# Kernel optimization log

Measured on AMD Instinct MI355X. Metric: run time of the kernel, lower is better.

The kernel has to match this reference:

```python
import jax, jax.numpy as jnp
import numpy as np

B, L, D, F = 4096, 200, 64, 100000


def setup_inputs() -> dict:
    key = jax.random.key(0)
    ks = jax.random.split(key, 12)
    film_hist = jax.random.randint(ks[0], (B, L), 0, F)                 # padded rated-film indices
    ratings = jax.random.uniform(ks[1], (B, L), jnp.float32) * 4.5 + 0.5  # letterboxd-style 0.5..5
    lengths = jax.random.randint(ks[2], (B,), 1, L + 1)                 # ragged history lengths (>=1)
    film_indices = jax.random.randint(ks[3], (B,), 0, F)                # target films to score
    emb_table = jax.random.normal(ks[4], (F, D), jnp.float32) * 0.1
    W1 = jax.random.normal(ks[5], (5 * D, 2 * D), jnp.float32) * 0.05
    b1 = jnp.zeros((2 * D,), jnp.float32)
    W2 = jax.random.normal(ks[6], (2 * D, D), jnp.float32) * 0.05
    b2 = jnp.zeros((D,), jnp.float32)
    W3 = jax.random.normal(ks[7], (D, 1), jnp.float32) * 0.05
    b3 = jnp.zeros((1,), jnp.float32)
    return {"film_hist": film_hist, "ratings": ratings, "lengths": lengths,
            "film_indices": film_indices, "emb_table": emb_table,
            "W1": W1, "b1": b1, "W2": W2, "b2": b2, "W3": W3, "b3": b3}


def _user_embeddings(film_hist, ratings, lengths, emb_table):
    # mask[b, l] = l < lengths[b]
    mask = jnp.arange(L)[None, :] < lengths[:, None]          # [B, L]
    n = lengths.astype(jnp.float32)                           # [B]
    mean_r = jnp.sum(jnp.where(mask, ratings, 0.0), axis=1) / n
    weights = ratings - mean_r[:, None] + 0.1                 # [B, L]
    hist_emb = emb_table[film_hist]                           # [B, L, D]
    w = hist_emb * weights[:, :, None]                        # weighted film embeddings
    m3 = mask[:, :, None]
    wmin = jnp.min(jnp.where(m3, w, jnp.inf), axis=1)
    wmax = jnp.max(jnp.where(m3, w, -jnp.inf), axis=1)
    wmean = jnp.sum(jnp.where(m3, w, 0.0), axis=1) / n[:, None]
    # median: sort valid entries (pads go to +inf at the end); torch.median
    # returns the lower middle element -> index (n-1)//2
    ws = jnp.sort(jnp.where(m3, w, jnp.inf), axis=1)
    mid = ((lengths - 1) // 2)[:, None, None]                 # [B,1,1]
    wmed = jnp.take_along_axis(ws, jnp.broadcast_to(mid, (B, 1, D)), axis=1)[:, 0, :]
    ue = jnp.concatenate([wmin, wmax, wmean, wmed], axis=1)   # [B, 4D]
    return ue / jnp.linalg.norm(ue, axis=1, keepdims=True)


def reference(film_hist, ratings, lengths, film_indices, emb_table, W1, b1, W2, b2, W3, b3):
    ue = _user_embeddings(film_hist, ratings, lengths, emb_table)  # [B, 4D]
    fe = emb_table[film_indices]                                   # [B, D]
    x = jnp.concatenate([ue, fe], axis=1)                          # [B, 5D]
    h = jax.nn.relu(x @ W1 + b1)   # Dropout(0.2) is identity in eval
    h = jax.nn.relu(h @ W2 + b2)
    return jax.nn.sigmoid(h @ W3 + b3)[:, 0]                       # [B]
```

## Files before the change

kernel.cpp:

```cpp
#include <hip/hip_runtime.h>
#include <hip/hip_bf16.h>
#include <stdint.h>


#define B_ 4096
#define L_ 200
#define D_ 64

__device__ __forceinline__ void xpose_sign(uint32_t (&W)[16]) {
  #define XS(k, jj, m) { uint32_t tt = ((W[k] ^ (W[(k)|(jj)] >> (jj))) & (m)); \
                         W[k] ^= tt; W[(k)|(jj)] ^= (tt << (jj)); }
  XS(0,8,0x00FF00FFu) XS(1,8,0x00FF00FFu) XS(2,8,0x00FF00FFu) XS(3,8,0x00FF00FFu)
  XS(4,8,0x00FF00FFu) XS(5,8,0x00FF00FFu) XS(6,8,0x00FF00FFu) XS(7,8,0x00FF00FFu)
  XS(0,4,0x0F0F0F0Fu) XS(1,4,0x0F0F0F0Fu) XS(2,4,0x0F0F0F0Fu) XS(3,4,0x0F0F0F0Fu)
  XS(8,4,0x0F0F0F0Fu) XS(9,4,0x0F0F0F0Fu) XS(10,4,0x0F0F0F0Fu) XS(11,4,0x0F0F0F0Fu)
  XS(0,2,0x33333333u) XS(1,2,0x33333333u) XS(4,2,0x33333333u) XS(5,2,0x33333333u)
  XS(8,2,0x33333333u) XS(9,2,0x33333333u) XS(12,2,0x33333333u) XS(13,2,0x33333333u)
  XS(0,1,0x55555555u) XS(2,1,0x55555555u) XS(4,1,0x55555555u) XS(6,1,0x55555555u)
  XS(8,1,0x55555555u) XS(10,1,0x55555555u) XS(12,1,0x55555555u) XS(14,1,0x55555555u)
  #undef XS
  const uint32_t S = W[0];
  W[0] = ~S;
  #pragma unroll
  for (int j = 1; j < 16; ++j) W[j] ^= S;
}

template<bool TWO>
__device__ __forceinline__ uint32_t select_med(
    const uint32_t (&W0)[16], const uint32_t (&W1x)[16],
    uint32_t a0, uint32_t a1, int k)
{
  uint32_t prefix = 0;
  #pragma unroll
  for (int bb = 15; bb >= 0; --bb) {
    const uint32_t z0 = a0 & ~W0[15 - bb];
    int cnt = __popc(z0);
    uint32_t z1 = 0u;
    if (TWO) {
      z1 = a1 & ~W1x[15 - bb];
      cnt += __popc(z1);
    }
    cnt += __builtin_amdgcn_update_dpp(0, cnt, 0xB1, 0xF, 0xF, true);
    cnt += __builtin_amdgcn_update_dpp(0, cnt, 0x4E, 0xF, 0xF, true);
    const bool zs = (k < cnt);
    a0 = zs ? z0 : (a0 ^ z0);
    if (TWO) a1 = zs ? z1 : (a1 ^ z1);
    k      = zs ? k : (k - cnt);
    prefix = zs ? prefix : (prefix | (1u << bb));
  }
  return prefix;
}

__global__ __launch_bounds__(256) void stats_kernel(
    const int* __restrict__ film_hist,
    const float* __restrict__ ratings,
    const int* __restrict__ lengths,
    const int* __restrict__ film_indices,
    const float* __restrict__ emb,
    float* __restrict__ x)
{
  __shared__ uint2 pair_s[L_];
  __shared__ float red[4];
  __shared__ float ue[4*D_];

  const int t = threadIdx.x;
  const int wv = t >> 6;
  const int lane = t & 63;
  const int d = t >> 2;
  const int sub = t & 3;
  const int b = blockIdx.x;
  const int n = lengths[b];

  const int fi = film_indices[b];
  const float fev = (t < 64) ? emb[(size_t)fi * D_ + t] : 0.f;

  float r = 0.f;
  if (t < n) {
    uint2 e;
    e.x = ((uint32_t)film_hist[(size_t)b*L_ + t]) << 8;
    const float rv = ratings[(size_t)b*L_ + t];
    e.y = __float_as_uint(rv);
    pair_s[t] = e;
    r = rv;
  }
  float s = r;
  #pragma unroll
  for (int off = 32; off; off >>= 1) s += __shfl_down(s, off);
  if (lane == 0) red[wv] = s;
  __syncthreads();
  const float mr1 = 0.1f - (red[0]+red[1]+red[2]+red[3]) / (float)n;

  const char* eb = (const char*)emb;
  const uint32_t d4 = (uint32_t)d * 4u;
  float vmin = __builtin_inff(), vmax = -__builtin_inff(), vsum = 0.f;
  uint32_t W0[16], W1x[16];
  #pragma unroll
  for (int j = 0; j < 16; ++j) { W0[j] = 0u; W1x[j] = 0u; }

  #pragma unroll
  for (int g = 0; g < 13; ++g) {
    if (16*g < n) {
      uint32_t kk[4];
      #pragma unroll
      for (int j = 0; j < 4; ++j) {
        const int l = sub + 16*g + 4*j;
        const int lc = (l < n) ? l : (n - 1);
        const uint2 e = pair_s[lc];
        const float w = *(const float*)(eb + (e.x + d4))
                        * (__uint_as_float(e.y) + mr1);
        vmin = fminf(vmin, (l < n) ? w :  __builtin_inff());
        vmax = fmaxf(vmax, (l < n) ? w : -__builtin_inff());
        vsum += (l < n) ? w : 0.f;
        kk[j] = __float_as_uint(w);
      }
      const uint32_t wA = __builtin_amdgcn_perm(kk[1], kk[0], 0x07060302u);
      const uint32_t wB = __builtin_amdgcn_perm(kk[3], kk[2], 0x07060302u);
      if (g < 8) { W0[2*g]       = wA; W0[2*g + 1]       = wB; }
      else       { W1x[2*(g-8)]  = wA; W1x[2*(g-8) + 1]  = wB; }
    }
  }

  vmin = fminf(vmin, __shfl_xor(vmin, 1));
  vmin = fminf(vmin, __shfl_xor(vmin, 2));
  vmax = fmaxf(vmax, __shfl_xor(vmax, 1));
  vmax = fmaxf(vmax, __shfl_xor(vmax, 2));
  vsum += __shfl_xor(vsum, 1);
  vsum += __shfl_xor(vsum, 2);

  const bool two = (n > 128);
  xpose_sign(W0);
  if (two) xpose_sign(W1x);

  const int cth = (n > sub) ? ((n - sub + 3) >> 2) : 0;
  const int v0 = (cth < 32) ? cth : 32;
  const int v1 = cth - v0;
  const int ce0 = (v0 + 1) >> 1, cf0 = v0 >> 1;
  uint32_t a0 = ((1u << ce0) - 1u) << (16 - ce0);
  if (cf0) a0 |= ((1u << cf0) - 1u) << (32 - cf0);
  const int ce1 = (v1 + 1) >> 1, cf1 = v1 >> 1;
  uint32_t a1 = ((1u << ce1) - 1u) << (16 - ce1);
  if (cf1) a1 |= ((1u << cf1) - 1u) << (32 - cf1);
  if (v1 == 0) a1 = 0u;

  const int k = (n - 1) >> 1;
  const uint32_t prefix = two ? select_med<true >(W0, W1x, a0, a1, k)
                              : select_med<false>(W0, W1x, a0, a1, k);

  if (sub == 0) {
    uint32_t key32 = (prefix << 16) | 0x8000u;
    const float med = (prefix & 0x8000u) ? __uint_as_float(key32 ^ 0x80000000u)
                                         : __uint_as_float(~key32);
    ue[d]       = vmin;
    ue[64 + d]  = vmax;
    ue[128 + d] = vsum / (float)n;
    ue[192 + d] = med;
  }
  __syncthreads();

  const float vv = ue[t];
  float ss = vv * vv;
  #pragma unroll
  for (int off = 32; off; off >>= 1) ss += __shfl_down(ss, off);
  if (lane == 0) red[wv] = ss;
  __syncthreads();
  const float rn = 1.0f / sqrtf(red[0]+red[1]+red[2]+red[3]);

  float* xb = x + (size_t)b * 320;
  xb[t] = vv * rn;
  if (t < 64) xb[256 + t] = fev;
}

#define U_ 4

__global__ __launch_bounds__(256) void mlp_kernel(
    const float* __restrict__ x,
    const float* __restrict__ W1, const float* __restrict__ b1,
    const float* __restrict__ W2, const float* __restrict__ b2,
    const float* __restrict__ W3, const float* __restrict__ b3,
    float* __restrict__ out)
{
  __shared__ float xs[U_*320];
  __shared__ float h1s[U_*128];
  __shared__ float h2s[U_*64];
  const int t = threadIdx.x;
  const int u0 = blockIdx.x * U_;

  for (int i = t; i < U_*80; i += 256)
    ((float4*)xs)[i] = ((const float4*)(x + (size_t)u0*320))[i];
  __syncthreads();

  {
    const int j = t & 127, g = t >> 7;
    const int ub = g*2;
    float acc[2];
    const float bj = b1[j];
    acc[0] = bj; acc[1] = bj;
    for (int i = 0; i < 320; i += 4) {
      float w0 = W1[(i+0)*128 + j];
      float w1 = W1[(i+1)*128 + j];
      float w2 = W1[(i+2)*128 + j];
      float w3 = W1[(i+3)*128 + j];
      #pragma unroll
      for (int q = 0; q < 2; ++q) {
        float4 xv = *(const float4*)&xs[(ub+q)*320 + i];
        acc[q] += xv.x*w0 + xv.y*w1 + xv.z*w2 + xv.w*w3;
      }
    }
    #pragma unroll
    for (int q = 0; q < 2; ++q) h1s[(ub+q)*128 + j] = fmaxf(acc[q], 0.f);
  }
  __syncthreads();

  {
    const int j = t & 63, g = t >> 6;
    float acc = b2[j];
    for (int i = 0; i < 128; i += 4) {
      float w0 = W2[(i+0)*64 + j];
      float w1 = W2[(i+1)*64 + j];
      float w2 = W2[(i+2)*64 + j];
      float w3 = W2[(i+3)*64 + j];
      float4 hv = *(const float4*)&h1s[g*128 + i];
      acc += hv.x*w0 + hv.y*w1 + hv.z*w2 + hv.w*w3;
    }
    h2s[g*64 + j] = fmaxf(acc, 0.f);
  }
  __syncthreads();

  if (t < U_*4) {
    const int u = t >> 2, sub = t & 3;
    float a = 0.f;
    #pragma unroll
    for (int i = 0; i < 16; ++i) a += h2s[u*64 + sub*16 + i] * W3[sub*16 + i];
    a += __shfl_xor(a, 1);
    a += __shfl_xor(a, 2);
    if (sub == 0) out[u0 + u] = 1.f / (1.f + __expf(-(a + b3[0])));
  }
}

extern "C" void kernel_launch(void* const* d_in, const int* in_sizes, int n_in,
                              void* d_out, int out_size, void* d_ws, size_t ws_size,
                              hipStream_t stream) {
  const int*   film_hist = (const int*)d_in[0];
  const float* ratings   = (const float*)d_in[1];
  const int*   lengths   = (const int*)d_in[2];
  const int*   film_idx  = (const int*)d_in[3];
  const float* emb       = (const float*)d_in[4];
  const float* W1 = (const float*)d_in[5];
  const float* b1 = (const float*)d_in[6];
  const float* W2 = (const float*)d_in[7];
  const float* b2 = (const float*)d_in[8];
  const float* W3 = (const float*)d_in[9];
  const float* b3 = (const float*)d_in[10];

  float* xbuf = (float*)d_ws;
  float* outp = (float*)d_out;

  stats_kernel<<<B_, 256, 0, stream>>>(film_hist, ratings, lengths, film_idx, emb, xbuf);
  mlp_kernel<<<B_/U_, 256, 0, stream>>>(xbuf, W1, b1, W2, b2, W3, b3, outp);
}
```

Baseline: 56.01 us.

## Software-pipeline embedding gathers in stats kernel and double MLP users per block

The stats kernel now pads the history pair buffer to a multiple of 16 with zero entries and folds the mean-rating offset into the stored weight once. The per-group gather loop becomes a two-stage software pipeline that issues the next group's global embedding loads before consuming the current group, with the bounds masking limited to the final partial group. Separately, the MLP kernel handles 8 users per block instead of 4, so each W1/W2 weight load is reused across more rows. The pipelining raises register pressure, and the larger MLP tile halves the number of blocks.

```diff
diff --git a/kernel.cpp b/kernel.cpp
--- a/kernel.cpp
+++ b/kernel.cpp
@@ -6,6 +6,7 @@
 #define B_ 4096
 #define L_ 200
 #define D_ 64
+#define LPAD 224
 
 __device__ __forceinline__ void xpose_sign(uint32_t (&W)[16]) {
   #define XS(k, jj, m) { uint32_t tt = ((W[k] ^ (W[(k)|(jj)] >> (jj))) & (m)); \
@@ -59,7 +60,7 @@
     const float* __restrict__ emb,
     float* __restrict__ x)
 {
-  __shared__ uint2 pair_s[L_];
+  __shared__ uint2 pair_s[LPAD];
   __shared__ float red[4];
   __shared__ float ue[4*D_];
 
@@ -75,13 +76,16 @@
   const float fev = (t < 64) ? emb[(size_t)fi * D_ + t] : 0.f;
 
   float r = 0.f;
-  if (t < n) {
+  if (t < LPAD) {
     uint2 e;
-    e.x = ((uint32_t)film_hist[(size_t)b*L_ + t]) << 8;
-    const float rv = ratings[(size_t)b*L_ + t];
-    e.y = __float_as_uint(rv);
+    if (t < n) {
+      e.x = ((uint32_t)film_hist[(size_t)b*L_ + t]) << 8;
+      r = ratings[(size_t)b*L_ + t];
+      e.y = __float_as_uint(r);
+    } else {
+      e.x = 0u; e.y = 0u;
+    }
     pair_s[t] = e;
-    r = rv;
   }
   float s = r;
   #pragma unroll
@@ -89,6 +93,9 @@
   if (lane == 0) red[wv] = s;
   __syncthreads();
   const float mr1 = 0.1f - (red[0]+red[1]+red[2]+red[3]) / (float)n;
+
+  if (t < n) pair_s[t].y = __float_as_uint(r + mr1);
+  __syncthreads();
 
   const char* eb = (const char*)emb;
   const uint32_t d4 = (uint32_t)d * 4u;
@@ -97,28 +104,60 @@
   #pragma unroll
   for (int j = 0; j < 16; ++j) { W0[j] = 0u; W1x[j] = 0u; }
 
-  #pragma unroll
-  for (int g = 0; g < 13; ++g) {
-    if (16*g < n) {
-      uint32_t kk[4];
-      #pragma unroll
-      for (int j = 0; j < 4; ++j) {
-        const int l = sub + 16*g + 4*j;
-        const int lc = (l < n) ? l : (n - 1);
-        const uint2 e = pair_s[lc];
-        const float w = *(const float*)(eb + (e.x + d4))
-                        * (__uint_as_float(e.y) + mr1);
-        vmin = fminf(vmin, (l < n) ? w :  __builtin_inff());
-        vmax = fmaxf(vmax, (l < n) ? w : -__builtin_inff());
-        vsum += (l < n) ? w : 0.f;
-        kk[j] = __float_as_uint(w);
-      }
-      const uint32_t wA = __builtin_amdgcn_perm(kk[1], kk[0], 0x07060302u);
-      const uint32_t wB = __builtin_amdgcn_perm(kk[3], kk[2], 0x07060302u);
-      if (g < 8) { W0[2*g]       = wA; W0[2*g + 1]       = wB; }
-      else       { W1x[2*(g-8)]  = wA; W1x[2*(g-8) + 1]  = wB; }
-    }
-  }
+  const int ng    = (n + 15) >> 4;
+  const int nfull = n >> 4;
+
+  #define LDSP(G, PE) { \
+    _Pragma("unroll") \
+    for (int j = 0; j < 4; ++j) PE[j] = pair_s[sub + 16*(G) + 4*j]; }
+  #define VMEMG(PE, EV) { \
+    _Pragma("unroll") \
+    for (int j = 0; j < 4; ++j) \
+      EV[j] = *(const float*)(eb + (PE[j].x + d4)); }
+  #define CONSG(G, EV, PE) { \
+    uint32_t kk[4]; \
+    _Pragma("unroll") \
+    for (int j = 0; j < 4; ++j) { \
+      const float w_ = EV[j] * __uint_as_float(PE[j].y); \
+      vsum += w_;                       \
+      kk[j] = __float_as_uint(w_); \
+    } \
+    if ((G) < nfull) { \
+      _Pragma("unroll") \
+      for (int j = 0; j < 4; ++j) { \
+        const float w_ = __uint_as_float(kk[j]); \
+        vmin = fminf(vmin, w_); vmax = fmaxf(vmax, w_); \
+      } \
+    } else { \
+      _Pragma("unroll") \
+      for (int j = 0; j < 4; ++j) { \
+        const int l_ = sub + 16*(G) + 4*j; \
+        const float w_ = __uint_as_float(kk[j]); \
+        vmin = fminf(vmin, (l_ < n) ? w_ :  __builtin_inff()); \
+        vmax = fmaxf(vmax, (l_ < n) ? w_ : -__builtin_inff()); \
+      } \
+    } \
+    const uint32_t wA_ = __builtin_amdgcn_perm(kk[1], kk[0], 0x07060302u); \
+    const uint32_t wB_ = __builtin_amdgcn_perm(kk[3], kk[2], 0x07060302u); \
+    if ((G) < 8) { W0[2*(G)]      = wA_; W0[2*(G)+1]      = wB_; } \
+    else         { W1x[2*((G)-8)] = wA_; W1x[2*((G)-8)+1] = wB_; } }
+
+  uint2 peA[4], peB[4];
+  float evA[4], evB[4];
+  LDSP(0, peA); VMEMG(peA, evA);
+  #pragma unroll
+  for (int gp = 0; gp < 7; ++gp) {
+    const int g = 2*gp;
+    if (g < ng) {
+      if (g+1 < ng) { LDSP(g+1, peB); VMEMG(peB, evB); }
+      CONSG(g, evA, peA);
+      if (g+2 < ng) { LDSP(g+2, peA); VMEMG(peA, evA); }
+      if (g+1 < ng) { CONSG(g+1, evB, peB); }
+    }
+  }
+  #undef LDSP
+  #undef VMEMG
+  #undef CONSG
 
   vmin = fminf(vmin, __shfl_xor(vmin, 1));
   vmin = fminf(vmin, __shfl_xor(vmin, 2));
@@ -170,7 +209,7 @@
   if (t < 64) xb[256 + t] = fev;
 }
 
-#define U_ 4
+#define U_ 8
 
 __global__ __launch_bounds__(256) void mlp_kernel(
     const float* __restrict__ x,
@@ -191,38 +230,46 @@
 
   {
     const int j = t & 127, g = t >> 7;
-    const int ub = g*2;
-    float acc[2];
+    const int ub = g*4;
+    float acc[4];
     const float bj = b1[j];
-    acc[0] = bj; acc[1] = bj;
+    #pragma unroll
+    for (int q = 0; q < 4; ++q) acc[q] = bj;
     for (int i = 0; i < 320; i += 4) {
       float w0 = W1[(i+0)*128 + j];
       float w1 = W1[(i+1)*128 + j];
       float w2 = W1[(i+2)*128 + j];
       float w3 = W1[(i+3)*128 + j];
       #pragma unroll
-      for (int q = 0; q < 2; ++q) {
+      for (int q = 0; q < 4; ++q) {
         float4 xv = *(const float4*)&xs[(ub+q)*320 + i];
         acc[q] += xv.x*w0 + xv.y*w1 + xv.z*w2 + xv.w*w3;
       }
     }
     #pragma unroll
-    for (int q = 0; q < 2; ++q) h1s[(ub+q)*128 + j] = fmaxf(acc[q], 0.f);
+    for (int q = 0; q < 4; ++q) h1s[(ub+q)*128 + j] = fmaxf(acc[q], 0.f);
   }
   __syncthreads();
 
   {
     const int j = t & 63, g = t >> 6;
-    float acc = b2[j];
+    const int ub = g*2;
+    float acc[2];
+    const float bj = b2[j];
+    acc[0] = bj; acc[1] = bj;
     for (int i = 0; i < 128; i += 4) {
       float w0 = W2[(i+0)*64 + j];
       float w1 = W2[(i+1)*64 + j];
       float w2 = W2[(i+2)*64 + j];
       float w3 = W2[(i+3)*64 + j];
-      float4 hv = *(const float4*)&h1s[g*128 + i];
-      acc += hv.x*w0 + hv.y*w1 + hv.z*w2 + hv.w*w3;
-    }
-    h2s[g*64 + j] = fmaxf(acc, 0.f);
+      #pragma unroll
+      for (int q = 0; q < 2; ++q) {
+        float4 hv = *(const float4*)&h1s[(ub+q)*128 + i];
+        acc[q] += hv.x*w0 + hv.y*w1 + hv.z*w2 + hv.w*w3;
+      }
+    }
+    #pragma unroll
+    for (int q = 0; q < 2; ++q) h2s[(ub+q)*64 + j] = fmaxf(acc[q], 0.f);
   }
   __syncthreads();
 
```

Result: faster. 52.82 us (-5.7%).
